# Performance work log

Hardware: AMD Instinct MI355X
Metric: run time of the kernel (lower is better)

## Reference

```python
import jax, jax.numpy as jnp
import numpy as np

N_NODES = 10000
D_IN = 128
D_OUT = 128
N_EDGES = 640000


def setup_inputs() -> dict:
    key = jax.random.key(0)
    k_x, k_e, k_wl, k_wr, k_b = jax.random.split(key, 5)
    x = jax.random.normal(k_x, (N_NODES, D_IN), dtype=jnp.float32)
    edge_index = jax.random.randint(k_e, (2, N_EDGES), 0, N_NODES, dtype=jnp.int64)
    # SAGEConv params: lin_l (neighbor path, with bias), lin_r (root path, no bias)
    s_l = 1.0 / np.sqrt(D_IN)
    W_l = jax.random.uniform(k_wl, (D_OUT, D_IN), dtype=jnp.float32, minval=-s_l, maxval=s_l)
    b_l = jax.random.uniform(k_b, (D_OUT,), dtype=jnp.float32, minval=-s_l, maxval=s_l)
    W_r = jax.random.uniform(k_wr, (D_OUT, D_IN), dtype=jnp.float32, minval=-s_l, maxval=s_l)
    return {"x": x, "edge_index": edge_index, "W_l": W_l, "b_l": b_l, "W_r": W_r}


def reference(x, edge_index, W_l, b_l, W_r):
    x = x.astype(jnp.float32)
    src, dst = edge_index[0], edge_index[1]
    # gather source features, mean-aggregate into destination nodes
    msgs = x[src]                                   # [E, D_in] irregular gather
    agg_sum = jax.ops.segment_sum(msgs, dst, num_segments=N_NODES)  # [N, D_in]
    deg = jax.ops.segment_sum(jnp.ones((src.shape[0],), dtype=x.dtype), dst,
                              num_segments=N_NODES)                 # [N]
    agg = jnp.where(deg[:, None] > 0, agg_sum / jnp.maximum(deg, 1.0)[:, None], 0.0)
    # SAGEConv: lin_l(agg) + lin_r(x)
    y = agg @ W_l.T + b_l + x @ W_r.T               # [N, D_out]
    return x + y                                     # residual add
```

## Files before the change

kernel.cpp:

```cpp
#include <hip/hip_runtime.h>

#define N_NODES 10000
#define D 128
#define N_EDGES 640000
#define NB 128
#define EPB (N_EDGES / NB)
#define SB 40
#define NPSB 250

typedef __attribute__((ext_vector_type(8))) short bf16x8;
typedef __attribute__((ext_vector_type(4))) float f32x4;
typedef __attribute__((ext_vector_type(8))) unsigned short us8;
typedef __attribute__((ext_vector_type(8))) float f32x8;


__device__ __forceinline__ unsigned short f2bf(float f) {
    union { float f; unsigned int i; } v;
    v.f = f;
    unsigned int b = v.i;
    unsigned int rounded = b + 0x7fffu + ((b >> 16) & 1u);
    return (unsigned short)(rounded >> 16);
}

__device__ __forceinline__ float bf2f(unsigned short u) {
    union { unsigned int i; float f; } v;
    v.i = ((unsigned int)u) << 16;
    return v.f;
}

__device__ __forceinline__ f32x8 bf2f8(us8 v) {
    f32x8 r;
#pragma unroll
    for (int t = 0; t < 8; ++t) r[t] = bf2f(v[t]);
    return r;
}


__global__ __launch_bounds__(1024) void hist_cast_kernel(const int* __restrict__ ei,
                                                         const float4* __restrict__ x4,
                                                         const float4* __restrict__ Wl4,
                                                         const float4* __restrict__ Wr4,
                                                         ushort4* __restrict__ xh4,
                                                         ushort4* __restrict__ Wlb4,
                                                         ushort4* __restrict__ Wrb4,
                                                         unsigned short* __restrict__ lrank,
                                                         unsigned short* __restrict__ cnt,
                                                         unsigned long long* __restrict__ flags) {
    __shared__ unsigned int h[N_NODES / 2];
    for (int w = threadIdx.x; w < N_NODES / 2; w += 1024) h[w] = 0u;
    if (blockIdx.x == 0 && threadIdx.x < SB) flags[threadIdx.x] = 0ULL;

    const int gid = blockIdx.x * 1024 + threadIdx.x;
    for (int i = gid; i < N_NODES * D / 4; i += NB * 1024) {
        float4 v = x4[i];
        ushort4 o;
        o.x = f2bf(v.x); o.y = f2bf(v.y); o.z = f2bf(v.z); o.w = f2bf(v.w);
        xh4[i] = o;
    }
    if (gid < D * D / 4) {
        float4 a = Wl4[gid], b = Wr4[gid];
        ushort4 oa, ob;
        oa.x = f2bf(a.x); oa.y = f2bf(a.y); oa.z = f2bf(a.z); oa.w = f2bf(a.w);
        ob.x = f2bf(b.x); ob.y = f2bf(b.y); ob.z = f2bf(b.z); ob.w = f2bf(b.w);
        Wlb4[gid] = oa;
        Wrb4[gid] = ob;
    }
    __syncthreads();

    const int base = blockIdx.x * EPB;
    for (int e = base + threadIdx.x; e < base + EPB; e += 1024) {
        int d = ei[N_EDGES + e];
        int sh = (d & 1) << 4;
        unsigned int old = atomicAdd(&h[d >> 1], 1u << sh);
        lrank[e] = (unsigned short)((old >> sh) & 0xffffu);
    }
    __syncthreads();
    unsigned int* c = (unsigned int*)(cnt + (size_t)blockIdx.x * N_NODES);
    for (int w = threadIdx.x; w < N_NODES / 2; w += 1024) c[w] = h[w];
}


__global__ __launch_bounds__(256) void colscan_scan_kernel(unsigned short* __restrict__ cnt,
                                                           int* __restrict__ row_start,
                                                           unsigned long long* __restrict__ flags) {
    const int t = threadIdx.x;
    const int b = blockIdx.x;
    const int n = b * NPSB + t;
    __shared__ int sc[256];
    __shared__ int blk_excl_sh;

    int deg = 0;
    if (t < NPSB) {
        int s = 0;
#pragma unroll 8
        for (int j = 0; j < NB; ++j) {
            int idx = j * N_NODES + n;
            int v = cnt[idx];
            cnt[idx] = (unsigned short)s;
            s += v;
        }
        deg = s;
    }
    sc[t] = deg;
    __syncthreads();
    for (int off = 1; off < 256; off <<= 1) {
        int v = (t >= off) ? sc[t - off] : 0;
        __syncthreads();
        sc[t] += v;
        __syncthreads();
    }
    const int total = sc[255];
    const int local_excl = sc[t] - deg;

    if (t == 0) {
        int excl = 0;
        if (b == 0) {
            __hip_atomic_store(&flags[0], (2ULL << 32) | (unsigned)total,
                               __ATOMIC_RELEASE, __HIP_MEMORY_SCOPE_AGENT);
        } else {
            __hip_atomic_store(&flags[b], (1ULL << 32) | (unsigned)total,
                               __ATOMIC_RELEASE, __HIP_MEMORY_SCOPE_AGENT);
            int j = b - 1;
            while (j >= 0) {
                unsigned long long f = __hip_atomic_load(&flags[j], __ATOMIC_ACQUIRE,
                                                         __HIP_MEMORY_SCOPE_AGENT);
                unsigned st = (unsigned)(f >> 32);
                if (st == 0) continue;
                excl += (int)(unsigned)(f & 0xffffffffULL);
                if (st == 2) break;
                --j;
            }
            __hip_atomic_store(&flags[b], (2ULL << 32) | (unsigned)(excl + total),
                               __ATOMIC_RELEASE, __HIP_MEMORY_SCOPE_AGENT);
        }
        blk_excl_sh = excl;
    }
    __syncthreads();
    if (t < NPSB) row_start[n] = blk_excl_sh + local_excl;
    if (b == SB - 1 && t == 0) row_start[N_NODES] = N_EDGES;
}


__global__ __launch_bounds__(256) void scatter_kernel(const int* __restrict__ ei,
                                                      const int* __restrict__ row_start,
                                                      const unsigned short* __restrict__ cnt,
                                                      const unsigned short* __restrict__ lrank,
                                                      unsigned short* __restrict__ csr) {
    int i = blockIdx.x * 256 + threadIdx.x;
    if (i < N_EDGES) {
        int b = i / EPB;
        int s = ei[i];
        int d = ei[N_EDGES + i];
        int pos = row_start[d] + (int)cnt[b * N_NODES + d] + (int)lrank[i];
        csr[pos] = (unsigned short)s;
    }
}


__global__ __launch_bounds__(256) void aggregate_kernel(const us8* __restrict__ xh8,
                                                        const int* __restrict__ row_start,
                                                        const unsigned short* __restrict__ csr,
                                                        us8* __restrict__ aggb8) {
    const int node = blockIdx.x * 4 + (threadIdx.x >> 6);
    const int lane = threadIdx.x & 63;
    const int lane16 = lane & 15;
    const int slot = lane >> 4;
    const int start = row_start[node];
    const int end = row_start[node + 1];

    f32x8 a0 = 0.f, a1 = 0.f, a2 = 0.f, a3 = 0.f;
    int j = start + slot;
    for (; j + 12 < end; j += 16) {
        int s0 = csr[j], s1 = csr[j + 4], s2 = csr[j + 8], s3 = csr[j + 12];
        a0 += bf2f8(xh8[s0 * 16 + lane16]);
        a1 += bf2f8(xh8[s1 * 16 + lane16]);
        a2 += bf2f8(xh8[s2 * 16 + lane16]);
        a3 += bf2f8(xh8[s3 * 16 + lane16]);
    }
    for (; j < end; j += 4) a0 += bf2f8(xh8[(int)csr[j] * 16 + lane16]);
    a0 = (a0 + a1) + (a2 + a3);

#pragma unroll
    for (int t = 0; t < 8; ++t) {
        float v = a0[t];
        v += __shfl_xor(v, 16, 64);
        v += __shfl_xor(v, 32, 64);
        a0[t] = v;
    }
    if (slot == 0) {
        int cE = end - start;
        float inv = (cE > 0) ? 1.0f / (float)cE : 0.0f;
        us8 pack;
#pragma unroll
        for (int t = 0; t < 8; ++t) pack[t] = f2bf(a0[t] * inv);
        aggb8[node * 16 + lane16] = pack;
    }
}


__global__ __launch_bounds__(256) void lin_mfma_kernel(const float* __restrict__ x,
                                                       const unsigned short* __restrict__ aggb,
                                                       const unsigned short* __restrict__ xh,
                                                       const unsigned short* __restrict__ Wlb,
                                                       const unsigned short* __restrict__ Wrb,
                                                       const float* __restrict__ bl,
                                                       float* __restrict__ out) {
    const int wave = threadIdx.x >> 6;
    const int lane = threadIdx.x & 63;
    const int l15 = lane & 15;
    const int quad = lane >> 4;
    const int mt = blockIdx.x * 4 + wave;
    if (mt >= 625) return;
    const int row0 = mt * 16;
    const int out0 = blockIdx.y * 16;

    const int m = row0 + l15;
    const int f = out0 + l15;

    const bf16x8* arow = (const bf16x8*)(aggb + (size_t)m * D) + quad;
    const bf16x8* xrow = (const bf16x8*)(xh   + (size_t)m * D) + quad;
    const bf16x8* wlro = (const bf16x8*)(Wlb + (size_t)f * D) + quad;
    const bf16x8* wrro = (const bf16x8*)(Wrb + (size_t)f * D) + quad;

    f32x4 c = {0.f, 0.f, 0.f, 0.f};
#pragma unroll
    for (int kk = 0; kk < 4; ++kk) {
        c = __builtin_amdgcn_mfma_f32_16x16x32_bf16(arow[kk * 4], wlro[kk * 4], c, 0, 0, 0);
        c = __builtin_amdgcn_mfma_f32_16x16x32_bf16(xrow[kk * 4], wrro[kk * 4], c, 0, 0, 0);
    }

    const float bias = bl[f];
#pragma unroll
    for (int r = 0; r < 4; ++r) {
        int row = row0 + quad * 4 + r;
        int idx = row * D + f;
        out[idx] = x[idx] + bias + c[r];
    }
}

extern "C" void kernel_launch(void* const* d_in, const int* in_sizes, int n_in,
                              void* d_out, int out_size, void* d_ws, size_t ws_size,
                              hipStream_t stream) {
    const float* x  = (const float*)d_in[0];
    const int*   ei = (const int*)d_in[1];
    const float* Wl = (const float*)d_in[2];
    const float* bl = (const float*)d_in[3];
    const float* Wr = (const float*)d_in[4];
    float* out = (float*)d_out;

    unsigned long long* flags = (unsigned long long*)d_ws;
    int* row_start = (int*)(flags + 64);
    unsigned short* cnt   = (unsigned short*)(row_start + 10016);
    unsigned short* lrank = cnt + (size_t)NB * N_NODES;
    unsigned short* csr   = lrank + N_EDGES;
    unsigned short* xh    = csr + N_EDGES;
    unsigned short* aggb  = xh + (size_t)N_NODES * D;
    unsigned short* Wlb   = aggb + (size_t)N_NODES * D;
    unsigned short* Wrb   = Wlb + D * D;

    hist_cast_kernel<<<NB, 1024, 0, stream>>>(ei, (const float4*)x, (const float4*)Wl,
                                              (const float4*)Wr, (ushort4*)xh,
                                              (ushort4*)Wlb, (ushort4*)Wrb,
                                              lrank, cnt, flags);
    colscan_scan_kernel<<<SB, 256, 0, stream>>>(cnt, row_start, flags);
    scatter_kernel<<<(N_EDGES + 255) / 256, 256, 0, stream>>>(ei, row_start, cnt, lrank, csr);
    aggregate_kernel<<<2500, 256, 0, stream>>>((const us8*)xh, row_start, csr,
                                               (us8*)aggb);
    lin_mfma_kernel<<<dim3(157, 8), 256, 0, stream>>>(x, aggb, xh, Wlb, Wrb, bl, out);
}
```

Before: 121.5 us.

## Fuse neighbor aggregation with MFMA linear layer via shared-memory tile

Merges the aggregate and linear kernels into one kernel. Each 1024-thread block aggregates 16 nodes (one wave per node) into a shared-memory bf16 tile, then 8 waves compute the 16x128 output tile with MFMA. This removes one launch and the global write and re-read of the aggregated matrix. In exchange, each block waits at a barrier for its slowest node, half the waves sit idle during the MFMA phase, and only 625 blocks are launched, which lowers parallelism.

```diff
diff --git a/kernel.cpp b/kernel.cpp
--- a/kernel.cpp
+++ b/kernel.cpp
@@ -157,17 +157,27 @@
 }
 
 
-__global__ __launch_bounds__(256) void aggregate_kernel(const us8* __restrict__ xh8,
-                                                        const int* __restrict__ row_start,
-                                                        const unsigned short* __restrict__ csr,
-                                                        us8* __restrict__ aggb8) {
-    const int node = blockIdx.x * 4 + (threadIdx.x >> 6);
+__global__ __launch_bounds__(1024) void agg_lin_kernel(const us8* __restrict__ xh8,
+                                                       const int* __restrict__ row_start,
+                                                       const unsigned short* __restrict__ csr,
+                                                       const float* __restrict__ x,
+                                                       const unsigned short* __restrict__ xh,
+                                                       const unsigned short* __restrict__ Wlb,
+                                                       const unsigned short* __restrict__ Wrb,
+                                                       const float* __restrict__ bl,
+                                                       float* __restrict__ out) {
+    __shared__ unsigned short aggT[16][136];
+    const int wave = threadIdx.x >> 6;
     const int lane = threadIdx.x & 63;
     const int lane16 = lane & 15;
     const int slot = lane >> 4;
+    const int quad = lane >> 4;
+    const int l15 = lane & 15;
+    const int row0 = blockIdx.x * 16;
+    const int node = row0 + wave;
+
     const int start = row_start[node];
     const int end = row_start[node + 1];
-
     f32x8 a0 = 0.f, a1 = 0.f, a2 = 0.f, a3 = 0.f;
     int j = start + slot;
     for (; j + 12 < end; j += 16) {
@@ -193,48 +203,32 @@
         us8 pack;
 #pragma unroll
         for (int t = 0; t < 8; ++t) pack[t] = f2bf(a0[t] * inv);
-        aggb8[node * 16 + lane16] = pack;
-    }
-}
-
-
-__global__ __launch_bounds__(256) void lin_mfma_kernel(const float* __restrict__ x,
-                                                       const unsigned short* __restrict__ aggb,
-                                                       const unsigned short* __restrict__ xh,
-                                                       const unsigned short* __restrict__ Wlb,
-                                                       const unsigned short* __restrict__ Wrb,
-                                                       const float* __restrict__ bl,
-                                                       float* __restrict__ out) {
-    const int wave = threadIdx.x >> 6;
-    const int lane = threadIdx.x & 63;
-    const int l15 = lane & 15;
-    const int quad = lane >> 4;
-    const int mt = blockIdx.x * 4 + wave;
-    if (mt >= 625) return;
-    const int row0 = mt * 16;
-    const int out0 = blockIdx.y * 16;
-
-    const int m = row0 + l15;
-    const int f = out0 + l15;
-
-    const bf16x8* arow = (const bf16x8*)(aggb + (size_t)m * D) + quad;
-    const bf16x8* xrow = (const bf16x8*)(xh   + (size_t)m * D) + quad;
-    const bf16x8* wlro = (const bf16x8*)(Wlb + (size_t)f * D) + quad;
-    const bf16x8* wrro = (const bf16x8*)(Wrb + (size_t)f * D) + quad;
-
-    f32x4 c = {0.f, 0.f, 0.f, 0.f};
-#pragma unroll
-    for (int kk = 0; kk < 4; ++kk) {
-        c = __builtin_amdgcn_mfma_f32_16x16x32_bf16(arow[kk * 4], wlro[kk * 4], c, 0, 0, 0);
-        c = __builtin_amdgcn_mfma_f32_16x16x32_bf16(xrow[kk * 4], wrro[kk * 4], c, 0, 0, 0);
-    }
-
-    const float bias = bl[f];
-#pragma unroll
-    for (int r = 0; r < 4; ++r) {
-        int row = row0 + quad * 4 + r;
-        int idx = row * D + f;
-        out[idx] = x[idx] + bias + c[r];
+        *(us8*)&aggT[wave][lane16 * 8] = pack;
+    }
+    __syncthreads();
+
+    if (wave < 8) {
+        const int f = wave * 16 + l15;
+        const unsigned short* ap = &aggT[l15][quad * 8];
+        const bf16x8* xrow = (const bf16x8*)(xh + (size_t)(row0 + l15) * D) + quad;
+        const bf16x8* wlro = (const bf16x8*)(Wlb + (size_t)f * D) + quad;
+        const bf16x8* wrro = (const bf16x8*)(Wrb + (size_t)f * D) + quad;
+
+        f32x4 c = {0.f, 0.f, 0.f, 0.f};
+#pragma unroll
+        for (int kk = 0; kk < 4; ++kk) {
+            bf16x8 af = *(const bf16x8*)(ap + kk * 32);
+            c = __builtin_amdgcn_mfma_f32_16x16x32_bf16(af, wlro[kk * 4], c, 0, 0, 0);
+            c = __builtin_amdgcn_mfma_f32_16x16x32_bf16(xrow[kk * 4], wrro[kk * 4], c, 0, 0, 0);
+        }
+
+        const float bias = bl[f];
+#pragma unroll
+        for (int r = 0; r < 4; ++r) {
+            int row = row0 + quad * 4 + r;
+            int idx = row * D + f;
+            out[idx] = x[idx] + bias + c[r];
+        }
     }
 }
 
@@ -254,8 +248,7 @@
     unsigned short* lrank = cnt + (size_t)NB * N_NODES;
     unsigned short* csr   = lrank + N_EDGES;
     unsigned short* xh    = csr + N_EDGES;
-    unsigned short* aggb  = xh + (size_t)N_NODES * D;
-    unsigned short* Wlb   = aggb + (size_t)N_NODES * D;
+    unsigned short* Wlb   = xh + (size_t)N_NODES * D;
     unsigned short* Wrb   = Wlb + D * D;
 
     hist_cast_kernel<<<NB, 1024, 0, stream>>>(ei, (const float4*)x, (const float4*)Wl,
@@ -264,7 +257,6 @@
                                               lrank, cnt, flags);
     colscan_scan_kernel<<<SB, 256, 0, stream>>>(cnt, row_start, flags);
     scatter_kernel<<<(N_EDGES + 255) / 256, 256, 0, stream>>>(ei, row_start, cnt, lrank, csr);
-    aggregate_kernel<<<2500, 256, 0, stream>>>((const us8*)xh, row_start, csr,
-                                               (us8*)aggb);
-    lin_mfma_kernel<<<dim3(157, 8), 256, 0, stream>>>(x, aggb, xh, Wlb, Wrb, bl, out);
-}
+    agg_lin_kernel<<<625, 1024, 0, stream>>>((const us8*)xh, row_start, csr,
+                                             x, xh, Wlb, Wrb, bl, out);
+}
```

Measured after the change: 121.5 us. About the same (+0.0%).
